# Performance work log

Hardware: AMD Instinct MI355X
Metric: run time of the kernel (lower is better)

## Reference

```python
import jax, jax.numpy as jnp
import numpy as np
from jax import lax


def conv2d(x, w, b, pad):
    out = lax.conv_general_dilated(x, w, (1, 1), [(pad, pad), (pad, pad)],
                                   dimension_numbers=('NCHW', 'OIHW', 'NCHW'))
    return out + b[None, :, None, None]


def deform_conv3x3(src, offset, weight, bias):
    # torchvision.ops.deform_conv2d, 3x3 kernel, stride 1, pad 1, no mask.
    # src [B,C,H,W]; offset [B,18,H,W] laid out (y,x) per kernel pos, row-major.
    B, C, H, W = src.shape
    off = offset.reshape(B, 9, 2, H, W)
    ky, kx = jnp.meshgrid(jnp.arange(3) - 1, jnp.arange(3) - 1, indexing='ij')
    ky = ky.reshape(9).astype(src.dtype)
    kx = kx.reshape(9).astype(src.dtype)
    yy = jnp.arange(H, dtype=src.dtype)[:, None]
    xx = jnp.arange(W, dtype=src.dtype)[None, :]
    py = yy[None, None] + ky[None, :, None, None] + off[:, :, 0]  # [B,9,H,W]
    px = xx[None, None] + kx[None, :, None, None] + off[:, :, 1]
    y0 = jnp.floor(py)
    x0 = jnp.floor(px)
    wy1 = py - y0
    wx1 = px - x0

    def gather(yi, xi):
        valid = ((yi >= 0) & (yi < H) & (xi >= 0) & (xi < W)).astype(src.dtype)
        yc = jnp.clip(yi, 0, H - 1).astype(jnp.int32)
        xc = jnp.clip(xi, 0, W - 1).astype(jnp.int32)
        vals = jax.vmap(lambda s, a, c: s[:, a, c])(src, yc, xc)  # [B,C,9,H,W]
        return vals * valid[:, None]

    sampled = (gather(y0, x0) * ((1 - wy1) * (1 - wx1))[:, None]
               + gather(y0, x0 + 1) * ((1 - wy1) * wx1)[:, None]
               + gather(y0 + 1, x0) * (wy1 * (1 - wx1))[:, None]
               + gather(y0 + 1, x0 + 1) * (wy1 * wx1)[:, None])
    wk = weight.reshape(weight.shape[0], weight.shape[1], 9)
    return jnp.einsum('bckhw,ock->bohw', sampled, wk) + bias[None, :, None, None]


def setup_inputs() -> dict:
    key = jax.random.key(0)
    ks = jax.random.split(key, 16)
    B, C, H, W, N = 1, 256, 96, 96, 8
    current_feat = jax.random.normal(ks[0], (B, C, H, W), dtype=jnp.float32)
    neighbor_feats = jax.random.normal(ks[1], (N, B, C, H, W), dtype=jnp.float32)
    coord_diffs = jax.random.normal(ks[2], (N, 4), dtype=jnp.float32)
    align_w = jax.random.normal(ks[3], (C, C, 3, 3), dtype=jnp.float32) * 0.02
    align_b = jax.random.normal(ks[4], (C,), dtype=jnp.float32) * 0.02
    offset_w = jax.random.normal(ks[5], (18, 2 * C, 3, 3), dtype=jnp.float32) * 0.002
    offset_b = jax.random.normal(ks[6], (18,), dtype=jnp.float32) * 0.002
    gate1_w = jax.random.normal(ks[7], (C // 2, 2 * C, 3, 3), dtype=jnp.float32) * 0.02
    gate1_b = jax.random.normal(ks[8], (C // 2,), dtype=jnp.float32) * 0.02
    gate2_w = jax.random.normal(ks[9], (1, C // 2, 1, 1), dtype=jnp.float32) * 0.02
    gate2_b = jax.random.normal(ks[10], (1,), dtype=jnp.float32) * 0.02
    enc_w = jax.random.normal(ks[11], (C, 4), dtype=jnp.float32) * 0.1
    enc_b = jax.random.normal(ks[12], (C,), dtype=jnp.float32) * 0.1
    return dict(current_feat=current_feat, neighbor_feats=neighbor_feats,
                coord_diffs=coord_diffs, align_w=align_w, align_b=align_b,
                offset_w=offset_w, offset_b=offset_b, gate1_w=gate1_w,
                gate1_b=gate1_b, gate2_w=gate2_w, gate2_b=gate2_b,
                enc_w=enc_w, enc_b=enc_b)


def reference(current_feat, neighbor_feats, coord_diffs, align_w, align_b,
              offset_w, offset_b, gate1_w, gate1_b, gate2_w, gate2_b,
              enc_w, enc_b):
    B, C, H, W = current_feat.shape
    N = neighbor_feats.shape[0]
    aligned = []
    for n in range(N):  # fixed small neighbor set (<= 8)
        src = neighbor_feats[n]
        concat = jnp.concatenate([src, current_feat], axis=1)  # [B,2C,H,W]
        offset = conv2d(concat, offset_w, offset_b, 1)         # [B,18,H,W]
        aligned.append(deform_conv3x3(src, offset, align_w, align_b))
    all_feats = jnp.stack(aligned, axis=1)                     # [B,N,C,H,W]
    # coordinate embedding: Linear(4 -> C) per neighbor, shaped [1,N,C,1,1]
    coord_embs = (coord_diffs @ enc_w.T + enc_b)[None, :, :, None, None]
    cur_exp = jnp.broadcast_to(current_feat[:, None], (B, N, C, H, W))
    energy = jnp.concatenate([cur_exp, all_feats], axis=2).reshape(B * N, 2 * C, H, W)
    g = jax.nn.relu(conv2d(energy, gate1_w, gate1_b, 1))
    g = jax.nn.sigmoid(conv2d(g, gate2_w, gate2_b, 0))          # [B*N,1,H,W]
    weights = jax.nn.softmax(g.reshape(B, N, 1, H, W), axis=1)
    fused = (all_feats * weights + coord_embs).sum(axis=1)      # [B,C,H,W]
    return current_feat + 0.5 * fused
```

## Files before the change

kernel.cpp:

```cpp
#include <hip/hip_runtime.h>
#include <math.h>

#define CH   256
#define HH   96
#define WW   96
#define NN   8
#define HWSZ 9216
#define PLANE (HWSZ*CH)

typedef unsigned short u16;
typedef unsigned int   u32;
typedef short bf16x8 __attribute__((ext_vector_type(8)));
typedef float f32x4  __attribute__((ext_vector_type(4)));

__device__ inline u16 f2bf(float f) {
    union { float f; u32 u; } v; v.f = f;
    u32 r = v.u + 0x7FFF + ((v.u >> 16) & 1);
    return (u16)(r >> 16);
}
__device__ inline float bflo(u32 u) {
    union { u32 u; float f; } v; v.u = u << 16; return v.f;
}
__device__ inline float bfhi(u32 u) {
    union { u32 u; float f; } v; v.u = u & 0xffff0000u; return v.f;
}
__device__ inline u32 pk2bf(float lo, float hi) {
    union { float f; u32 u; } a, b; a.f = lo; b.f = hi;
    u32 ra = a.u + 0x7FFF + ((a.u >> 16) & 1);
    u32 rb = b.u + 0x7FFF + ((b.u >> 16) & 1);
    return (ra >> 16) | (rb & 0xffff0000u);
}

__global__ void k_emb_sum(const float* __restrict__ cd,
                          const float* __restrict__ enc_w,
                          const float* __restrict__ enc_b,
                          float* __restrict__ emb)
{
    int c = threadIdx.x;
    float s = 0.f;
    for (int n = 0; n < NN; ++n) {
        float d = enc_b[c];
        #pragma unroll
        for (int j = 0; j < 4; ++j) d += cd[n*4 + j] * enc_w[c*4 + j];
        s += d;
    }
    emb[c] = s;
}

__global__ void k_to_nhwc(const float* __restrict__ in, u16* __restrict__ out)
{
    int n = blockIdx.y, c = threadIdx.x;
    int p0 = blockIdx.x * 192;
    const float* src = in + ((size_t)n * CH + c) * HWSZ + p0;
    u16* dst = out + (size_t)n * PLANE + (size_t)p0 * CH + c;
    for (int j = 0; j < 192; ++j)
        dst[(size_t)j * CH] = f2bf(src[j]);
}

__global__ void k_pack_w(const float* __restrict__ w, u16* __restrict__ wp,
                         int O, int O_pad, int CIN)
{
    int idx = blockIdx.x * 256 + threadIdx.x;
    int total = O_pad * CIN * 9;
    if (idx >= total) return;
    int o = idx / (CIN * 9);
    int K = idx % (CIN * 9);
    int tap = K / CIN, c = K % CIN;
    float v = (o < O) ? w[((size_t)o * CIN + c) * 9 + tap] : 0.f;
    int NKC = (CIN * 9) >> 5;
    int kc = K >> 5, kl = K & 31;
    int lane = (kl >> 3) * 16 + (o & 15);
    size_t dstp = (((size_t)(o >> 4) * NKC + kc) * 64 + lane) * 8 + (kl & 7);
    wp[dstp] = f2bf(v);
}

template<int MTW, int EPI>
__global__ __launch_bounds__(512) void k_conv_nhwc(
    const u16* __restrict__ in0, long s0,
    const u16* __restrict__ in1, long s1,
    const u16* __restrict__ Wp, const float* __restrict__ b1,
    const float* __restrict__ g2w, const float* __restrict__ g2b,
    float* __restrict__ out)
{
    constexpr int NKC = 144, NCC = 16;
    int n = blockIdx.x, t = blockIdx.y;
    int tx0 = (t % 3) * 32, ty0 = (t / 3) * 8;
    int tid = threadIdx.x, lane = tid & 63, w = tid >> 6;
    int mh = w >> 2, pg = w & 3;
    int colq = lane >> 4;

    __shared__ __align__(16) u16 SB[340*40];
    __shared__ float gpart[8][64];

    f32x4 acc[MTW][4];
    #pragma unroll
    for (int mt = 0; mt < MTW; ++mt)
        #pragma unroll
        for (int nf = 0; nf < 4; ++nf)
            acc[mt][nf] = (f32x4){0.f,0.f,0.f,0.f};

    int bidx[4];
    #pragma unroll
    for (int nf = 0; nf < 4; ++nf) {
        int px = pg*64 + nf*16 + (lane & 15);
        int row = px >> 5, col = px & 31;
        bidx[nf] = ((row+1)*34 + (col+1))*40 + colq*8;
    }

    for (int cc = 0; cc < NCC; ++cc) {
        const u16* base = (cc < 8) ? in0 + (size_t)n*s0 + cc*32
                                   : in1 + (size_t)n*s1 + (cc-8)*32;
        for (int i = tid; i < 1360; i += 512) {
            int ph = i >> 2, q = i & 3;
            int r = ph / 34, col = ph - r*34;
            int y = ty0 - 1 + r, x = tx0 - 1 + col;
            bool v = ((unsigned)y < (unsigned)HH) && ((unsigned)x < (unsigned)WW);
            int off = v ? (y*WW + x)*CH : 0;
            int4 val = *reinterpret_cast<const int4*>(base + off + q*8);
            if (!v) val = make_int4(0,0,0,0);
            *reinterpret_cast<int4*>(&SB[ph*40 + q*8]) = val;
        }
        __syncthreads();
        #pragma unroll
        for (int tap = 0; tap < 9; ++tap) {
            int kc = tap*NCC + cc;
            bf16x8 a[MTW];
            #pragma unroll
            for (int mt = 0; mt < MTW; ++mt)
                a[mt] = *reinterpret_cast<const bf16x8*>(
                    Wp + (((size_t)(mh*MTW+mt)*NKC + kc)*64 + lane)*8);
            const int dy = tap/3 - 1, dx = tap%3 - 1;
            #pragma unroll
            for (int nf = 0; nf < 4; ++nf) {
                bf16x8 b = *reinterpret_cast<const bf16x8*>(
                    &SB[bidx[nf] + (dy*34 + dx)*40]);
                #pragma unroll
                for (int mt = 0; mt < MTW; ++mt)
                    acc[mt][nf] = __builtin_amdgcn_mfma_f32_16x16x32_bf16(
                                      a[mt], b, acc[mt][nf], 0, 0, 0);
            }
        }
        __syncthreads();
    }

    if (EPI == 0) {
        #pragma unroll
        for (int nf = 0; nf < 4; ++nf) {
            int px = pg*64 + nf*16 + (lane & 15);
            int gp = (ty0 + (px>>5))*WW + tx0 + (px & 31);
            #pragma unroll
            for (int mt = 0; mt < MTW; ++mt) {
                int o_base = (mh*MTW+mt)*16 + colq*4;
                #pragma unroll
                for (int r = 0; r < 4; ++r) {
                    int o = o_base + r;
                    if (o < 18)
                        out[((size_t)n*18 + o)*HWSZ + gp] = acc[mt][nf][r] + b1[o];
                }
            }
        }
    } else {
        float part[4];
        #pragma unroll
        for (int nf = 0; nf < 4; ++nf) {
            float s = 0.f;
            #pragma unroll
            for (int mt = 0; mt < MTW; ++mt) {
                int o_base = (mh*MTW+mt)*16 + colq*4;
                #pragma unroll
                for (int r = 0; r < 4; ++r) {
                    int o = o_base + r;
                    float vv = fmaxf(acc[mt][nf][r] + b1[o], 0.f);
                    s += vv * g2w[o];
                }
            }
            part[nf] = s;
        }
        #pragma unroll
        for (int nf = 0; nf < 4; ++nf) {
            part[nf] += __shfl_xor(part[nf], 16, 64);
            part[nf] += __shfl_xor(part[nf], 32, 64);
        }
        if (lane < 16) {
            #pragma unroll
            for (int nf = 0; nf < 4; ++nf)
                gpart[w][nf*16 + lane] = part[nf];
        }
        __syncthreads();
        if (tid < 256) {
            int pxl = tid & 63, pgg = tid >> 6;
            float s = gpart[pgg][pxl] + gpart[4 + pgg][pxl] + g2b[0];
            float g = 1.f / (1.f + expf(-s));
            int px = pgg*64 + pxl;
            int gp = (ty0 + (px>>5))*WW + tx0 + (px & 31);
            out[(size_t)n*HWSZ + gp] = g;
        }
    }
}

__global__ __launch_bounds__(256) void k_deform_nhwc(
    const u16* __restrict__ nbrh, const float* __restrict__ offs,
    const u16* __restrict__ Wp, const float* __restrict__ ab,
    u16* __restrict__ alig)
{
    constexpr int NKC = 72;
    int n = blockIdx.x, t = blockIdx.y;
    int tx0 = (t % 3) * 32, ty0 = (t / 3) * 2;
    int tid = threadIdx.x, lane = tid & 63, w = tid >> 6;
    int colq = lane >> 4;

    __shared__ __align__(16) u16 pool[8448];
    __shared__ u32   cpos[576];
    __shared__ float cwy[576], cwx[576];
    u16* SB0 = pool;
    u16* SB1 = pool + 2560;

    const u16* src = nbrh + (size_t)n * PLANE;

    for (int i = tid; i < 576; i += 256) {
        int tt = i >> 6, px = i & 63;
        int y = ty0 + (px>>5), x = tx0 + (px & 31);
        int pp = y*WW + x;
        float oy = offs[((size_t)n*18 + 2*tt    )*HWSZ + pp];
        float ox = offs[((size_t)n*18 + 2*tt + 1)*HWSZ + pp];
        float py  = (float)y + (float)(tt/3 - 1) + oy;
        float pxx = (float)x + (float)(tt%3 - 1) + ox;
        py  = fminf(fmaxf(py,  -4.f), 100.f);
        pxx = fminf(fmaxf(pxx, -4.f), 100.f);
        float y0f = floorf(py), x0f = floorf(pxx);
        cpos[i] = ((u32)((int)y0f + 4) << 16) | (u32)((int)x0f + 4);
        cwy[i] = py - y0f; cwx[i] = pxx - x0f;
    }
    __syncthreads();

    f32x4 acc[4][4];
    #pragma unroll
    for (int mt = 0; mt < 4; ++mt)
        #pragma unroll
        for (int nf = 0; nf < 4; ++nf)
            acc[mt][nf] = (f32x4){0.f,0.f,0.f,0.f};

    int px = tid >> 2, chq = tid & 3;
    int sbw = px*40 + chq*8;
    int bb[4];
    #pragma unroll
    for (int nf = 0; nf < 4; ++nf)
        bb[nf] = (nf*16 + (lane & 15))*40 + colq*8;

    auto loadC = [&](int kc, int4* q) {
        int tt = kc >> 3, cc = kc & 7;
        int r = (tt<<6) + px;
        u32 cp = cpos[r];
        int y0 = (int)(cp >> 16) - 4, x0 = (int)(cp & 0xffff) - 4;
        bool y0i = (y0 >= 0) & (y0 < HH);
        bool y1i = (y0 >= -1) & (y0 < HH-1);
        bool x0i = (x0 >= 0) & (x0 < WW);
        bool x1i = (x0 >= -1) & (x0 < WW-1);
        int c0 = cc*32 + chq*8;
        int a00 = (y0*WW + x0)*CH + c0;
        int o00 = (y0i & x0i) ? a00            : 0;
        int o01 = (y0i & x1i) ? a00 + CH       : 0;
        int o10 = (y1i & x0i) ? a00 + WW*CH    : 0;
        int o11 = (y1i & x1i) ? a00 + WW*CH+CH : 0;
        int4 z = make_int4(0,0,0,0);
        int4 q0 = *reinterpret_cast<const int4*>(src + o00);
        int4 q1 = *reinterpret_cast<const int4*>(src + o01);
        int4 q2 = *reinterpret_cast<const int4*>(src + o10);
        int4 q3 = *reinterpret_cast<const int4*>(src + o11);
        q[0] = (y0i & x0i) ? q0 : z;
        q[1] = (y0i & x1i) ? q1 : z;
        q[2] = (y1i & x0i) ? q2 : z;
        q[3] = (y1i & x1i) ? q3 : z;
    };
    auto bilerp = [&](int kc, const int4* q) -> int4 {
        int r = ((kc >> 3)<<6) + px;
        float wy = cwy[r], wx = cwx[r];
        float w00 = (1.f-wy)*(1.f-wx), w01 = (1.f-wy)*wx;
        float w10 = wy*(1.f-wx),       w11 = wy*wx;
        int4 res;
        #pragma unroll
        for (int j = 0; j < 4; ++j) {
            u32 u00 = ((const u32*)&q[0])[j], u01 = ((const u32*)&q[1])[j];
            u32 u10 = ((const u32*)&q[2])[j], u11 = ((const u32*)&q[3])[j];
            float lo = w00*bflo(u00) + w01*bflo(u01) + w10*bflo(u10) + w11*bflo(u11);
            float hi = w00*bfhi(u00) + w01*bfhi(u01) + w10*bfhi(u10) + w11*bfhi(u11);
            ((u32*)&res)[j] = pk2bf(lo, hi);
        }
        return res;
    };
    auto loadA = [&](int kc, bf16x8* a) {
        #pragma unroll
        for (int mt = 0; mt < 4; ++mt)
            a[mt] = *reinterpret_cast<const bf16x8*>(
                Wp + (((size_t)(w*4+mt)*NKC + kc)*64 + lane)*8);
    };

    int4 crn[4];
    bf16x8 apf[4];
    loadC(0, crn);
    loadA(0, apf);
    int cur = 0;
    for (int kc = 0; kc < NKC; ++kc) {
        int4 vpk = bilerp(kc, crn);
        u16* SBc = cur ? SB1 : SB0;
        *reinterpret_cast<int4*>(&SBc[sbw]) = vpk;
        bf16x8 a4[4];
        #pragma unroll
        for (int mt = 0; mt < 4; ++mt) a4[mt] = apf[mt];
        if (kc + 1 < NKC) { loadC(kc + 1, crn); loadA(kc + 1, apf); }
        __syncthreads();
        #pragma unroll
        for (int nf = 0; nf < 4; ++nf) {
            bf16x8 b = *reinterpret_cast<const bf16x8*>(&SBc[bb[nf]]);
            #pragma unroll
            for (int mt = 0; mt < 4; ++mt)
                acc[mt][nf] = __builtin_amdgcn_mfma_f32_16x16x32_bf16(
                                  a4[mt], b, acc[mt][nf], 0, 0, 0);
        }
        cur ^= 1;
    }

    __syncthreads();
    u16* TO = pool;
    u16* aligp = alig + (size_t)n * PLANE;
    #pragma unroll
    for (int h = 0; h < 2; ++h) {
        #pragma unroll
        for (int sub = 0; sub < 2; ++sub) {
            int nf = 2*h + sub;
            int pl = sub*16 + (lane & 15);
            #pragma unroll
            for (int mt = 0; mt < 4; ++mt) {
                int o = (w*4+mt)*16 + colq*4;
                ushort4 v;
                v.x = f2bf(acc[mt][nf][0] + ab[o]);
                v.y = f2bf(acc[mt][nf][1] + ab[o+1]);
                v.z = f2bf(acc[mt][nf][2] + ab[o+2]);
                v.w = f2bf(acc[mt][nf][3] + ab[o+3]);
                *reinterpret_cast<ushort4*>(&TO[pl*264 + o]) = v;
            }
        }
        __syncthreads();
        #pragma unroll
        for (int it = 0; it < 4; ++it) {
            int i = tid + it*256;
            int pr = i >> 5, ck = i & 31;
            int nf = 2*h + (pr >> 4);
            int pxx = nf*16 + (pr & 15);
            int gp = (ty0 + (pxx>>5))*WW + tx0 + (pxx & 31);
            *reinterpret_cast<int4*>(aligp + (size_t)gp*CH + ck*8) =
                *reinterpret_cast<const int4*>(&TO[pr*264 + ck*8]);
        }
        __syncthreads();
    }
}

__global__ __launch_bounds__(256) void k_fuse_nhwc(
    const float* __restrict__ cur, const u16* __restrict__ alig,
    const float* __restrict__ g, const float* __restrict__ emb,
    float* __restrict__ out)
{
    int p0 = blockIdx.x * 32;
    int tid = threadIdx.x;
    __shared__ float wE[NN][32];
    __shared__ float trans[256][33];

    if (tid < 32) {
        int p = p0 + tid;
        float e[NN], m = -1e30f;
        #pragma unroll
        for (int n = 0; n < NN; ++n) { e[n] = g[n*HWSZ + p]; m = fmaxf(m, e[n]); }
        float se = 0.f;
        #pragma unroll
        for (int n = 0; n < NN; ++n) { e[n] = expf(e[n] - m); se += e[n]; }
        float inv = 1.f / se;
        #pragma unroll
        for (int n = 0; n < NN; ++n) wE[n][tid] = e[n] * inv;
    }
    __syncthreads();

    #pragma unroll
    for (int it = 0; it < 4; ++it) {
        int i = tid + it*256;
        int px = i >> 5, ck = i & 31;
        float a8[8];
        #pragma unroll
        for (int j = 0; j < 8; ++j) a8[j] = 0.f;
        #pragma unroll
        for (int n = 0; n < NN; ++n) {
            int4 v = *reinterpret_cast<const int4*>(
                &alig[((size_t)n*HWSZ + p0 + px)*CH + ck*8]);
            float f = wE[n][px];
            #pragma unroll
            for (int j4 = 0; j4 < 4; ++j4) {
                u32 u = ((const u32*)&v)[j4];
                a8[2*j4]   += bflo(u) * f;
                a8[2*j4+1] += bfhi(u) * f;
            }
        }
        #pragma unroll
        for (int j = 0; j < 8; ++j) {
            int c = ck*8 + j;
            trans[c][px ^ (c & 31)] = a8[j] + emb[c];
        }
    }
    __syncthreads();
    for (int it = 0; it < 32; ++it) {
        int c = (tid >> 5) + it*8, px = tid & 31;
        int idx = c*HWSZ + p0 + px;
        out[idx] = cur[idx] + 0.5f * trans[c][px ^ (c & 31)];
    }
}

extern "C" void kernel_launch(void* const* d_in, const int* in_sizes, int n_in,
                              void* d_out, int out_size, void* d_ws, size_t ws_size,
                              hipStream_t stream)
{
    const float* cur = (const float*)d_in[0];
    const float* nbr = (const float*)d_in[1];
    const float* cd  = (const float*)d_in[2];
    const float* aw  = (const float*)d_in[3];
    const float* ab  = (const float*)d_in[4];
    const float* ow  = (const float*)d_in[5];
    const float* ob  = (const float*)d_in[6];
    const float* g1w = (const float*)d_in[7];
    const float* g1b = (const float*)d_in[8];
    const float* g2w = (const float*)d_in[9];
    const float* g2b = (const float*)d_in[10];
    const float* ew  = (const float*)d_in[11];
    const float* eb  = (const float*)d_in[12];
    float* out = (float*)d_out;
    float* ws  = (float*)d_ws;

    float* offs = ws;
    float* gbuf = offs + 1327104;
    float* emb  = gbuf + 73728;
    u16* nbrh = (u16*)(emb + 256);
    u16* curh = nbrh + (size_t)NN*PLANE;
    u16* alig = curh + PLANE;
    u16* wpO  = alig + (size_t)NN*PLANE;
    u16* wpG  = wpO + 147456;
    u16* wpA  = wpG + 589824;

    k_emb_sum<<<dim3(1), dim3(256), 0, stream>>>(cd, ew, eb, emb);
    k_to_nhwc<<<dim3(48, 8), dim3(256), 0, stream>>>(nbr, nbrh);
    k_to_nhwc<<<dim3(48, 1), dim3(256), 0, stream>>>(cur, curh);
    k_pack_w<<<dim3((32*4608 + 255)/256), dim3(256), 0, stream>>>(ow, wpO, 18, 32, 512);
    k_pack_w<<<dim3((128*4608 + 255)/256), dim3(256), 0, stream>>>(g1w, wpG, 128, 128, 512);
    k_pack_w<<<dim3((256*2304 + 255)/256), dim3(256), 0, stream>>>(aw, wpA, 256, 256, 256);

    k_conv_nhwc<1, 0><<<dim3(8, 36), dim3(512), 0, stream>>>(
        nbrh, (long)PLANE, curh, 0L, wpO, ob, nullptr, nullptr, offs);
    k_deform_nhwc<<<dim3(8, 144), dim3(256), 0, stream>>>(nbrh, offs, wpA, ab, alig);
    k_conv_nhwc<4, 1><<<dim3(8, 36), dim3(512), 0, stream>>>(
        curh, 0L, alig, (long)PLANE, wpG, g1b, g2w, g2b, gbuf);
    k_fuse_nhwc<<<dim3(288), dim3(256), 0, stream>>>(cur, alig, gbuf, emb, out);
}
```

Before: 434.1 us.

## Tile NCHW->NHWC transpose via LDS and precompute deform gather offsets/weights

The NCHW-to-NHWC bf16 conversion now reads float4 rows into a shared-memory tile and writes 16-byte NHWC chunks. Previously each thread did strided 2-byte stores. The deformable conv precomputes per-tap clamped corner offsets and masked bilinear weights in LDS, which removes the per-iteration bounds checks and selects. It also remaps threads so each wave gathers one 8-channel slice per pixel, and does the bilinear math with packed float2 operations. The new LDS B-tile layout has no padding, so it risks bank conflicts on MFMA operand reads.

```diff
diff --git a/kernel.cpp b/kernel.cpp
--- a/kernel.cpp
+++ b/kernel.cpp
@@ -12,6 +12,7 @@
 typedef unsigned int   u32;
 typedef short bf16x8 __attribute__((ext_vector_type(8)));
 typedef float f32x4  __attribute__((ext_vector_type(4)));
+typedef float f32x2  __attribute__((ext_vector_type(2)));
 
 __device__ inline u16 f2bf(float f) {
     union { float f; u32 u; } v; v.f = f;
@@ -47,14 +48,31 @@
     emb[c] = s;
 }
 
-__global__ void k_to_nhwc(const float* __restrict__ in, u16* __restrict__ out)
-{
-    int n = blockIdx.y, c = threadIdx.x;
-    int p0 = blockIdx.x * 192;
-    const float* src = in + ((size_t)n * CH + c) * HWSZ + p0;
-    u16* dst = out + (size_t)n * PLANE + (size_t)p0 * CH + c;
-    for (int j = 0; j < 192; ++j)
-        dst[(size_t)j * CH] = f2bf(src[j]);
+__global__ __launch_bounds__(256) void k_to_nhwc(const float* __restrict__ in,
+                                                 u16* __restrict__ out)
+{
+    int n = blockIdx.y;
+    int p0 = blockIdx.x * 64;
+    int tid = threadIdx.x;
+    __shared__ u16 T[64][262];
+
+    int px4 = (tid & 15) * 4, cb = tid >> 4;
+    for (int it = 0; it < 16; ++it) {
+        int c = cb + it*16;
+        float4 v = *reinterpret_cast<const float4*>(
+            in + ((size_t)n*CH + c)*HWSZ + p0 + px4);
+        T[px4+0][c] = f2bf(v.x);
+        T[px4+1][c] = f2bf(v.y);
+        T[px4+2][c] = f2bf(v.z);
+        T[px4+3][c] = f2bf(v.w);
+    }
+    __syncthreads();
+    int pxb = tid >> 5, ck = tid & 31;
+    for (int it = 0; it < 8; ++it) {
+        int p = pxb + it*8;
+        *reinterpret_cast<int4*>(out + (size_t)n*PLANE + (size_t)(p0+p)*CH + ck*8) =
+            *reinterpret_cast<const int4*>(&T[p][ck*8]);
+    }
 }
 
 __global__ void k_pack_w(const float* __restrict__ w, u16* __restrict__ wp,
@@ -209,17 +227,17 @@
     int tid = threadIdx.x, lane = tid & 63, w = tid >> 6;
     int colq = lane >> 4;
 
-    __shared__ __align__(16) u16 pool[8448];
-    __shared__ u32   cpos[576];
-    __shared__ float cwy[576], cwx[576];
-    u16* SB0 = pool;
-    u16* SB1 = pool + 2560;
+    __shared__ __align__(16) char pool[26624];
+    u16*    SB0  = (u16*)pool;
+    u16*    SB1  = SB0 + 2048;
+    int4*   cofs = (int4*)(pool + 8192);
+    float4* cwt  = (float4*)(pool + 17408);
 
     const u16* src = nbrh + (size_t)n * PLANE;
 
     for (int i = tid; i < 576; i += 256) {
-        int tt = i >> 6, px = i & 63;
-        int y = ty0 + (px>>5), x = tx0 + (px & 31);
+        int tt = i >> 6, p = i & 63;
+        int y = ty0 + (p>>5), x = tx0 + (p & 31);
         int pp = y*WW + x;
         float oy = offs[((size_t)n*18 + 2*tt    )*HWSZ + pp];
         float ox = offs[((size_t)n*18 + 2*tt + 1)*HWSZ + pp];
@@ -228,8 +246,24 @@
         py  = fminf(fmaxf(py,  -4.f), 100.f);
         pxx = fminf(fmaxf(pxx, -4.f), 100.f);
         float y0f = floorf(py), x0f = floorf(pxx);
-        cpos[i] = ((u32)((int)y0f + 4) << 16) | (u32)((int)x0f + 4);
-        cwy[i] = py - y0f; cwx[i] = pxx - x0f;
+        int y0 = (int)y0f, x0 = (int)x0f;
+        float wy = py - y0f, wx = pxx - x0f;
+        bool b00 = (y0 >= 0)  & (y0 < HH)   & (x0 >= 0)  & (x0 < WW);
+        bool b01 = (y0 >= 0)  & (y0 < HH)   & (x0 >= -1) & (x0 < WW-1);
+        bool b10 = (y0 >= -1) & (y0 < HH-1) & (x0 >= 0)  & (x0 < WW);
+        bool b11 = (y0 >= -1) & (y0 < HH-1) & (x0 >= -1) & (x0 < WW-1);
+        int a00 = (y0*WW + x0)*CH;
+        int4 o4;
+        o4.x = b00 ? a00             : 0;
+        o4.y = b01 ? a00 + CH        : 0;
+        o4.z = b10 ? a00 + WW*CH     : 0;
+        o4.w = b11 ? a00 + WW*CH+CH  : 0;
+        float4 w4;
+        w4.x = b00 ? (1.f-wy)*(1.f-wx) : 0.f;
+        w4.y = b01 ? (1.f-wy)*wx       : 0.f;
+        w4.z = b10 ? wy*(1.f-wx)       : 0.f;
+        w4.w = b11 ? wy*wx             : 0.f;
+        cofs[i] = o4; cwt[i] = w4;
     }
     __syncthreads();
 
@@ -240,74 +274,70 @@
         for (int nf = 0; nf < 4; ++nf)
             acc[mt][nf] = (f32x4){0.f,0.f,0.f,0.f};
 
-    int px = tid >> 2, chq = tid & 3;
-    int sbw = px*40 + chq*8;
+    int sbw = ((lane>>4)*4 + w)*128 + (lane&15)*8;
     int bb[4];
     #pragma unroll
     for (int nf = 0; nf < 4; ++nf)
-        bb[nf] = (nf*16 + (lane & 15))*40 + colq*8;
-
-    auto loadC = [&](int kc, int4* q) {
-        int tt = kc >> 3, cc = kc & 7;
-        int r = (tt<<6) + px;
-        u32 cp = cpos[r];
-        int y0 = (int)(cp >> 16) - 4, x0 = (int)(cp & 0xffff) - 4;
-        bool y0i = (y0 >= 0) & (y0 < HH);
-        bool y1i = (y0 >= -1) & (y0 < HH-1);
-        bool x0i = (x0 >= 0) & (x0 < WW);
-        bool x1i = (x0 >= -1) & (x0 < WW-1);
-        int c0 = cc*32 + chq*8;
-        int a00 = (y0*WW + x0)*CH + c0;
-        int o00 = (y0i & x0i) ? a00            : 0;
-        int o01 = (y0i & x1i) ? a00 + CH       : 0;
-        int o10 = (y1i & x0i) ? a00 + WW*CH    : 0;
-        int o11 = (y1i & x1i) ? a00 + WW*CH+CH : 0;
-        int4 z = make_int4(0,0,0,0);
-        int4 q0 = *reinterpret_cast<const int4*>(src + o00);
-        int4 q1 = *reinterpret_cast<const int4*>(src + o01);
-        int4 q2 = *reinterpret_cast<const int4*>(src + o10);
-        int4 q3 = *reinterpret_cast<const int4*>(src + o11);
-        q[0] = (y0i & x0i) ? q0 : z;
-        q[1] = (y0i & x1i) ? q1 : z;
-        q[2] = (y1i & x0i) ? q2 : z;
-        q[3] = (y1i & x1i) ? q3 : z;
+        bb[nf] = (nf*4 + colq)*128 + (lane&15)*8;
+
+    int4 o4; float4 w4;
+    int4 crn[4];
+    bf16x8 apf[4];
+
+    auto loadC = [&](int kc) {
+        int c0 = (kc & 7)*32 + w*8;
+        crn[0] = *reinterpret_cast<const int4*>(src + o4.x + c0);
+        crn[1] = *reinterpret_cast<const int4*>(src + o4.y + c0);
+        crn[2] = *reinterpret_cast<const int4*>(src + o4.z + c0);
+        crn[3] = *reinterpret_cast<const int4*>(src + o4.w + c0);
     };
-    auto bilerp = [&](int kc, const int4* q) -> int4 {
-        int r = ((kc >> 3)<<6) + px;
-        float wy = cwy[r], wx = cwx[r];
-        float w00 = (1.f-wy)*(1.f-wx), w01 = (1.f-wy)*wx;
-        float w10 = wy*(1.f-wx),       w11 = wy*wx;
+    auto loadA = [&](int kc) {
+        #pragma unroll
+        for (int mt = 0; mt < 4; ++mt)
+            apf[mt] = *reinterpret_cast<const bf16x8*>(
+                Wp + (((size_t)(w*4+mt)*NKC + kc)*64 + lane)*8);
+    };
+    auto bilerp = [&](float4 wt, const int4* q) -> int4 {
+        f32x2 W00 = {wt.x, wt.x}, W01 = {wt.y, wt.y};
+        f32x2 W10 = {wt.z, wt.z}, W11 = {wt.w, wt.w};
         int4 res;
         #pragma unroll
         for (int j = 0; j < 4; ++j) {
             u32 u00 = ((const u32*)&q[0])[j], u01 = ((const u32*)&q[1])[j];
             u32 u10 = ((const u32*)&q[2])[j], u11 = ((const u32*)&q[3])[j];
-            float lo = w00*bflo(u00) + w01*bflo(u01) + w10*bflo(u10) + w11*bflo(u11);
-            float hi = w00*bfhi(u00) + w01*bfhi(u01) + w10*bfhi(u10) + w11*bfhi(u11);
-            ((u32*)&res)[j] = pk2bf(lo, hi);
+            f32x2 c00 = {bflo(u00), bfhi(u00)};
+            f32x2 c01 = {bflo(u01), bfhi(u01)};
+            f32x2 c10 = {bflo(u10), bfhi(u10)};
+            f32x2 c11 = {bflo(u11), bfhi(u11)};
+            f32x2 v = c00*W00;
+            v += c01*W01;
+            v += c10*W10;
+            v += c11*W11;
+            ((u32*)&res)[j] = pk2bf(v.x, v.y);
         }
         return res;
     };
-    auto loadA = [&](int kc, bf16x8* a) {
-        #pragma unroll
-        for (int mt = 0; mt < 4; ++mt)
-            a[mt] = *reinterpret_cast<const bf16x8*>(
-                Wp + (((size_t)(w*4+mt)*NKC + kc)*64 + lane)*8);
-    };
-
-    int4 crn[4];
-    bf16x8 apf[4];
-    loadC(0, crn);
-    loadA(0, apf);
+
+    o4 = cofs[lane]; w4 = cwt[lane];
+    loadC(0);
+    loadA(0);
     int cur = 0;
     for (int kc = 0; kc < NKC; ++kc) {
-        int4 vpk = bilerp(kc, crn);
+        int4 vpk = bilerp(w4, crn);
         u16* SBc = cur ? SB1 : SB0;
         *reinterpret_cast<int4*>(&SBc[sbw]) = vpk;
         bf16x8 a4[4];
         #pragma unroll
         for (int mt = 0; mt < 4; ++mt) a4[mt] = apf[mt];
-        if (kc + 1 < NKC) { loadC(kc + 1, crn); loadA(kc + 1, apf); }
+        int kn = kc + 1;
+        if (kn < NKC) {
+            if ((kn & 7) == 0) {
+                int r = (kn >> 3)*64 + lane;
+                o4 = cofs[r]; w4 = cwt[r];
+            }
+            loadC(kn);
+            loadA(kn);
+        }
         __syncthreads();
         #pragma unroll
         for (int nf = 0; nf < 4; ++nf) {
@@ -321,7 +351,7 @@
     }
 
     __syncthreads();
-    u16* TO = pool;
+    u16* TO = (u16*)pool;
     u16* aligp = alig + (size_t)n * PLANE;
     #pragma unroll
     for (int h = 0; h < 2; ++h) {
@@ -443,8 +473,8 @@
     u16* wpA  = wpG + 589824;
 
     k_emb_sum<<<dim3(1), dim3(256), 0, stream>>>(cd, ew, eb, emb);
-    k_to_nhwc<<<dim3(48, 8), dim3(256), 0, stream>>>(nbr, nbrh);
-    k_to_nhwc<<<dim3(48, 1), dim3(256), 0, stream>>>(cur, curh);
+    k_to_nhwc<<<dim3(144, 8), dim3(256), 0, stream>>>(nbr, nbrh);
+    k_to_nhwc<<<dim3(144, 1), dim3(256), 0, stream>>>(cur, curh);
     k_pack_w<<<dim3((32*4608 + 255)/256), dim3(256), 0, stream>>>(ow, wpO, 18, 32, 512);
     k_pack_w<<<dim3((128*4608 + 255)/256), dim3(256), 0, stream>>>(g1w, wpG, 128, 128, 512);
     k_pack_w<<<dim3((256*2304 + 255)/256), dim3(256), 0, stream>>>(aw, wpA, 256, 256, 256);
```

Measured after the change: 435.0 us. About the same (+0.2%).
